# Optimization experiments

Hardware: AMD Instinct MI355X
Metric: run time of the kernel (lower is better)

The kernel has to match this reference:

```python
import jax, jax.numpy as jnp
import numpy as np

DIM_IN = 16
DIM_OUT = 64

def setup_inputs() -> dict:
    key = jax.random.key(0)
    ks = jax.random.split(key, 7)
    B, T, N = 4, 8, 256
    s_in = 1.0 / np.sqrt(DIM_IN)
    s_out = 1.0 / np.sqrt(DIM_OUT)
    return {
        "query": jax.random.normal(ks[0], (B, N, DIM_IN), dtype=jnp.float32),
        "keys": jax.random.normal(ks[1], (B, T, N, DIM_IN), dtype=jnp.float32),
        "Wq": jax.random.uniform(ks[2], (DIM_IN, DIM_OUT), jnp.float32, -s_in, s_in),
        "bq": jax.random.uniform(ks[3], (DIM_OUT,), jnp.float32, -s_in, s_in),
        "Wk": jax.random.uniform(ks[4], (DIM_IN, DIM_OUT), jnp.float32, -s_in, s_in),
        "bk": jax.random.uniform(ks[5], (DIM_OUT,), jnp.float32, -s_in, s_in),
        "wt": jax.random.uniform(ks[6], (DIM_OUT,), jnp.float32, -s_out, s_out),
    }

def reference(query, keys, Wq, bq, Wk, bk, wt):
    # q: [B, N, D] -> [B, 1, N, 1, D]
    q = (jnp.einsum('bnf,fd->bnd', query, Wq) + bq)[:, None, :, None, :]
    # k: [B, T, N, D] -> [B, T, 1, N, D]
    k = (jnp.einsum('btnf,fd->btnd', keys, Wk) + bk)[:, :, None, :, :]
    # scores: [B, T, N, N] via tanh of broadcast add, reduced by wt
    scores = jnp.einsum('btnmd,d->btnm', jnp.tanh(q + k), wt)
    return jax.nn.softmax(scores, axis=-1)
```

## Files before the change

kernel.cpp:

```cpp
#include <hip/hip_runtime.h>

#define B_ 4
#define T_ 8
#define N_ 256
#define F_ 16
#define D_ 64
#define NP (D_/2)
#define CHUNK 8
#define NCH (N_/CHUNK)

#define SC 2.8853900817779268f
#define LOG2E 1.4426950408889634f

typedef __attribute__((ext_vector_type(16))) float f32x16;

__device__ __forceinline__ float fast_exp2(float x) { return __builtin_amdgcn_exp2f(x); }
__device__ __forceinline__ float fast_rcp(float x)  { return __builtin_amdgcn_rcpf(x); }

__global__ __launch_bounds__(256)
void tattn_proj_kernel(const float* __restrict__ query,
                       const float* __restrict__ keys,
                       const float* __restrict__ Wq, const float* __restrict__ bq,
                       const float* __restrict__ Wk, const float* __restrict__ bk,
                       float* __restrict__ Eq, float* __restrict__ EkT)
{
    const int tid = threadIdx.x;
    const int row = blockIdx.x * 4 + (tid >> 6);
    const int j   = tid & 63;
    const int NQ  = B_ * N_;

    if (row < NQ) {
        const float* in = query + (size_t)row * F_;
        float acc = bq[j];
        #pragma unroll
        for (int f = 0; f < F_; ++f) acc = fmaf(in[f], Wq[f * D_ + j], acc);
        Eq[(size_t)row * D_ + j] = fast_exp2(acc * SC);
    } else {
        const int r  = row - NQ;
        const int bt = r >> 8, n = r & (N_ - 1);
        const float* in = keys + (size_t)r * F_;
        float acc = bk[j];
        #pragma unroll
        for (int f = 0; f < F_; ++f) acc = fmaf(in[f], Wk[f * D_ + j], acc);
        EkT[((size_t)bt * D_ + j) * N_ + n] = fast_exp2(acc * SC);
    }
}

__global__ __launch_bounds__(256, 3)
void tattn_main_kernel(const float* __restrict__ Eq,
                       const float* __restrict__ EkT,
                       const float* __restrict__ wt,
                       float* __restrict__ out)
{
    __shared__ float pbuf[CHUNK][N_];
    __shared__ float wls[D_];
    __shared__ float totL[CHUNK];

    const int tid = threadIdx.x;
    const int bid = blockIdx.x;
    const int ch  = bid % NCH;
    const int t   = (bid / NCH) % T_;
    const int b   = bid / (NCH * T_);
    const int n0  = ch * CHUNK;
    const int bt  = b * T_ + t;

    if (tid < D_) wls[tid] = 2.0f * wt[tid];

    float kreg[D_];
    {
        const float* kp = EkT + (size_t)bt * D_ * N_ + tid;
        #pragma unroll
        for (int d = 0; d < D_; ++d) kreg[d] = kp[(size_t)d * N_];
    }
    __syncthreads();

    float wv[D_];
    #pragma unroll
    for (int d = 0; d < D_; d += 4) {
        float4 v = *reinterpret_cast<const float4*>(&wls[d]);
        wv[d] = v.x; wv[d+1] = v.y; wv[d+2] = v.z; wv[d+3] = v.w;
    }
    float Wsum = 0.f;
    #pragma unroll
    for (int d = 0; d < D_; ++d) Wsum += wv[d];
    Wsum *= 0.5f;

    const float* eqrow = Eq + ((size_t)(b * N_ + n0)) * D_;

    #pragma unroll 1
    for (int nn = 0; nn < CHUNK; ++nn) {
        f32x16 e0, e1, e2, e3;
        asm volatile("s_load_dwordx16 %0, %4, 0x0\n\t"
                     "s_load_dwordx16 %1, %4, 0x40\n\t"
                     "s_load_dwordx16 %2, %4, 0x80\n\t"
                     "s_load_dwordx16 %3, %4, 0xc0"
                     : "=&s"(e0), "=&s"(e1), "=&s"(e2), "=&s"(e3)
                     : "s"(eqrow));
        asm volatile("s_waitcnt lgkmcnt(0)"
                     : "+s"(e0), "+s"(e1), "+s"(e2), "+s"(e3));
        __builtin_amdgcn_sched_barrier(0);

        float a0 = 0.f, a1 = 0.f, a2 = 0.f, a3 = 0.f;
        #pragma unroll
        for (int pr = 0; pr < NP; ++pr) {
            float eqa, eqb;
            if      (pr <  8) { eqa = e0[2*pr];      eqb = e0[2*pr+1];      }
            else if (pr < 16) { eqa = e1[2*pr-16];   eqb = e1[2*pr-15];     }
            else if (pr < 24) { eqa = e2[2*pr-32];   eqb = e2[2*pr-31];     }
            else              { eqa = e3[2*pr-48];   eqb = e3[2*pr-47];     }
            float pA = fmaf(eqa, kreg[2*pr+0], 1.0f);
            float qA = fmaf(eqb, kreg[2*pr+1], 1.0f);
            float nA = fmaf(wv[2*pr+1], pA, wv[2*pr] * qA);
            float r  = fast_rcp(pA * qA);
            if      ((pr & 3) == 0) a0 = fmaf(nA, r, a0);
            else if ((pr & 3) == 1) a1 = fmaf(nA, r, a1);
            else if ((pr & 3) == 2) a2 = fmaf(nA, r, a2);
            else                    a3 = fmaf(nA, r, a3);
        }
        float score = Wsum - ((a0 + a1) + (a2 + a3));

        pbuf[nn][tid] = fast_exp2(score * LOG2E);
        eqrow += D_;
    }
    __syncthreads();

    const int lane = tid & 63;
    const int wid  = tid >> 6;
    #pragma unroll
    for (int rr = 0; rr < 2; ++rr) {
        const int row = wid * 2 + rr;
        float4 v = *reinterpret_cast<const float4*>(&pbuf[row][lane * 4]);
        float s = (v.x + v.y) + (v.z + v.w);
        #pragma unroll
        for (int off = 32; off >= 1; off >>= 1) s += __shfl_xor(s, off);
        if (lane == 0) totL[row] = s;
    }
    __syncthreads();

    const size_t obase = ((size_t)(bt * N_ + n0)) * N_ + tid;
    #pragma unroll
    for (int nn = 0; nn < CHUNK; ++nn)
        out[obase + (size_t)nn * N_] = pbuf[nn][tid] * fast_rcp(totL[nn]);
}

extern "C" void kernel_launch(void* const* d_in, const int* in_sizes, int n_in,
                              void* d_out, int out_size, void* d_ws, size_t ws_size,
                              hipStream_t stream) {
    const float* query = (const float*)d_in[0];
    const float* keys  = (const float*)d_in[1];
    const float* Wq    = (const float*)d_in[2];
    const float* bq    = (const float*)d_in[3];
    const float* Wk    = (const float*)d_in[4];
    const float* bk    = (const float*)d_in[5];
    const float* wt    = (const float*)d_in[6];
    float* out = (float*)d_out;

    float* Eq  = (float*)d_ws;
    float* EkT = Eq + (size_t)B_ * N_ * D_;

    const int rows = B_ * N_ + B_ * T_ * N_;
    hipLaunchKernelGGL(tattn_proj_kernel, dim3(rows / 4), dim3(256), 0, stream,
                       query, keys, Wq, bq, Wk, bk, Eq, EkT);

    hipLaunchKernelGGL(tattn_main_kernel, dim3(B_ * T_ * NCH), dim3(256), 0, stream,
                       Eq, EkT, wt, out);
}
```

Measured before the change: 30.78 us.

## Interleave weights with Eq in scalar stream and double-buffer SMEM scalar loads

```diff
diff --git a/kernel.cpp b/kernel.cpp
--- a/kernel.cpp
+++ b/kernel.cpp
@@ -22,7 +22,9 @@
                        const float* __restrict__ keys,
                        const float* __restrict__ Wq, const float* __restrict__ bq,
                        const float* __restrict__ Wk, const float* __restrict__ bk,
-                       float* __restrict__ Eq, float* __restrict__ EkT)
+                       const float* __restrict__ wt,
+                       float* __restrict__ StreamQ, float* __restrict__ EkT,
+                       float* __restrict__ hdr)
 {
     const int tid = threadIdx.x;
     const int row = blockIdx.x * 4 + (tid >> 6);
@@ -34,7 +36,18 @@
         float acc = bq[j];
         #pragma unroll
         for (int f = 0; f < F_; ++f) acc = fmaf(in[f], Wq[f * D_ + j], acc);
-        Eq[(size_t)row * D_ + j] = fast_exp2(acc * SC);
+        float eq = fast_exp2(acc * SC);
+        float* qs = StreamQ + (size_t)row * (4 * NP);
+        const int pr = j >> 1;
+        const float w2l = 2.0f * LOG2E * wt[j];
+        if ((j & 1) == 0) { qs[4*pr + 0] = eq; qs[4*pr + 2] = w2l; }
+        else              { qs[4*pr + 1] = eq; qs[4*pr + 3] = w2l; }
+        if (row == 0) {
+            float w = wt[j];
+            #pragma unroll
+            for (int off = 32; off >= 1; off >>= 1) w += __shfl_xor(w, off);
+            if (j == 0) hdr[0] = w * LOG2E;
+        }
     } else {
         const int r  = row - NQ;
         const int bt = r >> 8, n = r & (N_ - 1);
@@ -46,14 +59,13 @@
     }
 }
 
-__global__ __launch_bounds__(256, 3)
-void tattn_main_kernel(const float* __restrict__ Eq,
+__global__ __launch_bounds__(256, 4)
+void tattn_main_kernel(const float* __restrict__ StreamQ,
                        const float* __restrict__ EkT,
-                       const float* __restrict__ wt,
+                       const float* __restrict__ hdr,
                        float* __restrict__ out)
 {
     __shared__ float pbuf[CHUNK][N_];
-    __shared__ float wls[D_];
     __shared__ float totL[CHUNK];
 
     const int tid = threadIdx.x;
@@ -64,64 +76,65 @@
     const int n0  = ch * CHUNK;
     const int bt  = b * T_ + t;
 
-    if (tid < D_) wls[tid] = 2.0f * wt[tid];
-
     float kreg[D_];
     {
         const float* kp = EkT + (size_t)bt * D_ * N_ + tid;
         #pragma unroll
         for (int d = 0; d < D_; ++d) kreg[d] = kp[(size_t)d * N_];
     }
-    __syncthreads();
 
-    float wv[D_];
-    #pragma unroll
-    for (int d = 0; d < D_; d += 4) {
-        float4 v = *reinterpret_cast<const float4*>(&wls[d]);
-        wv[d] = v.x; wv[d+1] = v.y; wv[d+2] = v.z; wv[d+3] = v.w;
+    const float WsumL = *hdr;
+    const float* srow = StreamQ + ((size_t)(b * N_ + n0)) * (4 * NP);
+
+    f32x16 cA0, cA1, cB0, cB1;
+    float ac0 = 0.f, ac1 = 0.f, ac2 = 0.f, ac3 = 0.f;
+
+    asm volatile("s_load_dwordx16 %0, %2, 0x0\n\t"
+                 "s_load_dwordx16 %1, %2, 0x40"
+                 : "=&s"(cA0), "=&s"(cA1) : "s"(srow));
+
+#define STEP(C0, C1, X0, X1, KK)                                              \
+    {                                                                         \
+        asm volatile("s_waitcnt lgkmcnt(0)" : "+s"(C0), "+s"(C1));            \
+        if ((KK) + 1 < 32) {                                                  \
+            asm volatile("s_load_dwordx16 %0, %2, 0x0\n\t"                    \
+                         "s_load_dwordx16 %1, %2, 0x40"                       \
+                         : "=&s"(X0), "=&s"(X1)                               \
+                         : "s"(srow + ((KK) + 1) * 32));                      \
+        }                                                                     \
+        __builtin_amdgcn_sched_barrier(0);                                    \
+        if (((KK) & 3) == 0) { ac0 = 0.f; ac1 = 0.f; ac2 = 0.f; ac3 = 0.f; }  \
+        _Pragma("unroll")                                                     \
+        for (int i = 0; i < 8; ++i) {                                         \
+            const int pr = ((KK) & 3) * 8 + i;                                \
+            float ea = (i < 4) ? C0[4*i+0] : C1[4*(i-4)+0];                   \
+            float eb = (i < 4) ? C0[4*i+1] : C1[4*(i-4)+1];                   \
+            float W0 = (i < 4) ? C0[4*i+2] : C1[4*(i-4)+2];                   \
+            float W1 = (i < 4) ? C0[4*i+3] : C1[4*(i-4)+3];                   \
+            float pA = fmaf(ea, kreg[2*pr+0], 1.0f);                          \
+            float qA = fmaf(eb, kreg[2*pr+1], 1.0f);                          \
+            float nA = fmaf(W0, qA, W1 * pA);                                 \
+            float r  = fast_rcp(pA * qA);                                     \
+            if      (i == 0 || i == 4) ac0 = fmaf(nA, r, ac0);                \
+            else if (i == 1 || i == 5) ac1 = fmaf(nA, r, ac1);                \
+            else if (i == 2 || i == 6) ac2 = fmaf(nA, r, ac2);                \
+            else                       ac3 = fmaf(nA, r, ac3);                \
+        }                                                                     \
+        if (((KK) & 3) == 3)                                                  \
+            pbuf[(KK) >> 2][tid] =                                            \
+                fast_exp2(WsumL - ((ac0 + ac1) + (ac2 + ac3)));               \
     }
-    float Wsum = 0.f;
-    #pragma unroll
-    for (int d = 0; d < D_; ++d) Wsum += wv[d];
-    Wsum *= 0.5f;
 
-    const float* eqrow = Eq + ((size_t)(b * N_ + n0)) * D_;
+#define ROW(R)                                  \
+    STEP(cA0, cA1, cB0, cB1, (R)*4 + 0)         \
+    STEP(cB0, cB1, cA0, cA1, (R)*4 + 1)         \
+    STEP(cA0, cA1, cB0, cB1, (R)*4 + 2)         \
+    STEP(cB0, cB1, cA0, cA1, (R)*4 + 3)
 
-    #pragma unroll 1
-    for (int nn = 0; nn < CHUNK; ++nn) {
-        f32x16 e0, e1, e2, e3;
-        asm volatile("s_load_dwordx16 %0, %4, 0x0\n\t"
-                     "s_load_dwordx16 %1, %4, 0x40\n\t"
-                     "s_load_dwordx16 %2, %4, 0x80\n\t"
-                     "s_load_dwordx16 %3, %4, 0xc0"
-                     : "=&s"(e0), "=&s"(e1), "=&s"(e2), "=&s"(e3)
-                     : "s"(eqrow));
-        asm volatile("s_waitcnt lgkmcnt(0)"
-                     : "+s"(e0), "+s"(e1), "+s"(e2), "+s"(e3));
-        __builtin_amdgcn_sched_barrier(0);
+    ROW(0) ROW(1) ROW(2) ROW(3) ROW(4) ROW(5) ROW(6) ROW(7)
+#undef ROW
+#undef STEP
 
-        float a0 = 0.f, a1 = 0.f, a2 = 0.f, a3 = 0.f;
-        #pragma unroll
-        for (int pr = 0; pr < NP; ++pr) {
-            float eqa, eqb;
-            if      (pr <  8) { eqa = e0[2*pr];      eqb = e0[2*pr+1];      }
-            else if (pr < 16) { eqa = e1[2*pr-16];   eqb = e1[2*pr-15];     }
-            else if (pr < 24) { eqa = e2[2*pr-32];   eqb = e2[2*pr-31];     }
-            else              { eqa = e3[2*pr-48];   eqb = e3[2*pr-47];     }
-            float pA = fmaf(eqa, kreg[2*pr+0], 1.0f);
-            float qA = fmaf(eqb, kreg[2*pr+1], 1.0f);
-            float nA = fmaf(wv[2*pr+1], pA, wv[2*pr] * qA);
-            float r  = fast_rcp(pA * qA);
-            if      ((pr & 3) == 0) a0 = fmaf(nA, r, a0);
-            else if ((pr & 3) == 1) a1 = fmaf(nA, r, a1);
-            else if ((pr & 3) == 2) a2 = fmaf(nA, r, a2);
-            else                    a3 = fmaf(nA, r, a3);
-        }
-        float score = Wsum - ((a0 + a1) + (a2 + a3));
-
-        pbuf[nn][tid] = fast_exp2(score * LOG2E);
-        eqrow += D_;
-    }
     __syncthreads();
 
     const int lane = tid & 63;
@@ -155,13 +168,14 @@
     const float* wt    = (const float*)d_in[6];
     float* out = (float*)d_out;
 
-    float* Eq  = (float*)d_ws;
-    float* EkT = Eq + (size_t)B_ * N_ * D_;
+    float* StreamQ = (float*)d_ws;
+    float* EkT     = StreamQ + (size_t)B_ * N_ * 4 * NP;
+    float* hdr     = EkT + (size_t)B_ * T_ * D_ * N_;
 
     const int rows = B_ * N_ + B_ * T_ * N_;
     hipLaunchKernelGGL(tattn_proj_kernel, dim3(rows / 4), dim3(256), 0, stream,
-                       query, keys, Wq, bq, Wk, bk, Eq, EkT);
+                       query, keys, Wq, bq, Wk, bk, wt, StreamQ, EkT, hdr);
 
     hipLaunchKernelGGL(tattn_main_kernel, dim3(B_ * T_ * NCH), dim3(256), 0, stream,
-                       Eq, EkT, wt, out);
+                       StreamQ, EkT, hdr, out);
 }
```

After: 34.72 us. +12.8%, slower.
